# Optimization experiments

Measured on AMD Instinct MI355X. Metric: run time of the kernel, lower is better.

Reference implementation:

```python
import jax, jax.numpy as jnp
import numpy as np

B, T, D = 8, 1024, 512
H = 8
F_OUT = D // H          # 64 per head
ALPHA = 0.2             # LeakyReLU slope in GAT
MASK_RATE = 0.3
GAMMA = 0.0625          # DistanceAdj gamma
BIAS = 0.2              # DistanceAdj bias
LN_EPS = 1e-5
NEG_INF = -9e15
L2_EPS = 1e-12          # F.normalize eps


def setup_inputs() -> dict:
    key = jax.random.key(0)
    ks = jax.random.split(key, 8)
    return {
        "x": jax.random.normal(ks[0], (B, T, D), jnp.float32),
        "W": jax.random.normal(ks[1], (H, D, F_OUT), jnp.float32) * 0.05,
        "a_src": jax.random.normal(ks[2], (H, F_OUT), jnp.float32) * 0.05,
        "a_dst": jax.random.normal(ks[3], (H, F_OUT), jnp.float32) * 0.05,
        "W2": jax.random.normal(ks[4], (D, D), jnp.float32) * 0.02,
        "b2": jnp.zeros((D,), jnp.float32),
        "ln_g": jnp.ones((D,), jnp.float32),
        "ln_b": jnp.zeros((D,), jnp.float32),
    }


def _distance_adj(batch, t):
    # DistanceAdj: Gaussian kernel over temporal index distance, shared across batch
    idx = jnp.arange(t, dtype=jnp.float32)
    d2 = (idx[:, None] - idx[None, :]) ** 2
    adj = jnp.exp(-GAMMA * d2 - BIAS)                      # [T, T]
    return jnp.broadcast_to(adj[None], (batch, t, t))      # [B, T, T]


def reference(x, W, a_src, a_dst, W2, b2, ln_g, ln_b):
    b, t, d = x.shape
    adj = _distance_adj(b, t)

    # top-k magnitude node selection -> row/col union mask (index_fill loop)
    k = int(MASK_RATE * t)
    mags = jnp.linalg.norm(x, axis=2)                      # [B, T]
    _, topk = jax.lax.top_k(mags, k)                       # [B, k]
    sel = jnp.zeros((b, t), bool).at[jnp.arange(b)[:, None], topk].set(True)
    mask = sel[:, :, None] | sel[:, None, :]               # rows OR cols filled
    adj = jnp.where(mask, adj, 0.0)

    # GAT multi-head attention (dense masked form, dropout=0 at eval)
    Wh = jnp.einsum("btd,hdf->bhtf", x, W)                 # [B,H,T,F']
    e_src = jnp.einsum("bhtf,hf->bht", Wh, a_src)
    e_dst = jnp.einsum("bhtf,hf->bht", Wh, a_dst)
    e = jax.nn.leaky_relu(e_src[..., :, None] + e_dst[..., None, :], ALPHA)
    e = jnp.where(adj[:, None] > 0, e, NEG_INF)            # masked logits
    attn = jax.nn.softmax(e, axis=-1)                      # [B,H,T,T]
    hp = jnp.einsum("bhts,bhsf->bhtf", attn, Wh)
    hp = jax.nn.elu(hp)                                    # concat=True -> elu per head
    tmp = hp.transpose(0, 2, 1, 3).reshape(b, t, d)        # concat heads -> [B,T,512]

    # signed-sqrt + F.normalize (default dim=1 -> over T axis)
    tmp = jnp.sqrt(jax.nn.relu(tmp)) - jnp.sqrt(jax.nn.relu(-tmp))
    nrm = jnp.linalg.norm(tmp, axis=1, keepdims=True)      # [B,1,D]
    tmp = tmp / jnp.maximum(nrm, L2_EPS)

    # residual linear + LayerNorm + permute
    y = x + tmp @ W2 + b2
    mu = jnp.mean(y, axis=-1, keepdims=True)
    var = jnp.mean((y - mu) ** 2, axis=-1, keepdims=True)
    y = (y - mu) / jnp.sqrt(var + LN_EPS) * ln_g + ln_b
    return y.transpose(0, 2, 1)                            # [B, D, T]
```

## Files before the change

### kernel.cpp

```cpp
#include <hip/hip_runtime.h>
#include <hip/hip_bf16.h>

typedef unsigned short u16;
typedef short bf16x8 __attribute__((ext_vector_type(8)));
typedef float f32x4 __attribute__((ext_vector_type(4)));
typedef int   i32x4 __attribute__((ext_vector_type(4)));

#define NB 8
#define NT 1024
#define ND 512
#define KSEL 307
#define PSTR 152
#define TSTR 136

__device__ __forceinline__ float bf2f(u16 u){
  union { unsigned int i; float f; } c; c.i = ((unsigned int)u) << 16; return c.f;
}
__device__ __forceinline__ u16 f2bf(float f){
  __hip_bfloat16 h = __float2bfloat16(f);
  u16 u; __builtin_memcpy(&u, &h, 2); return u;
}

__global__ void k_convert_w(const float* __restrict__ W, const float* __restrict__ W2,
                            u16* __restrict__ WcatT, u16* __restrict__ W2T){
  int idx = blockIdx.x * 256 + threadIdx.x;
  if (idx < 262144){
    int c = idx >> 9, d = idx & 511;
    int src = ((c >> 6) << 15) | (d << 6) | (c & 63);
    WcatT[idx] = f2bf(W[src]);
  } else {
    int i = idx - 262144;
    int n = i >> 9, k = i & 511;
    W2T[i] = f2bf(W2[(k << 9) | n]);
  }
}

__global__ void k_select(const float* __restrict__ mags, int* __restrict__ sel){
  __shared__ float sm[NT];
  int b = blockIdx.x;
  int tid = threadIdx.x;
  for (int i = tid; i < NT; i += 256) sm[i] = mags[b * NT + i];
  __syncthreads();
  int tl = tid >> 2, tq = tid & 3;
  int t = blockIdx.y * 64 + tl;
  float m = sm[t];
  int cnt = 0;
  int s0 = tq * 256;
  for (int s = s0; s < s0 + 256; s++){
    float v = sm[s];
    cnt += (v > m) || (v == m && s < t);
  }
  cnt += __shfl_xor(cnt, 1, 64);
  cnt += __shfl_xor(cnt, 2, 64);
  if (tq == 0) sel[b * NT + t] = (cnt < KSEL) ? 1 : 0;
}

__launch_bounds__(256)
__global__ void k_gemm_wh(const float* __restrict__ x, const u16* __restrict__ Bt,
                          const float* __restrict__ a_src, const float* __restrict__ a_dst,
                          u16* __restrict__ WhT, float* __restrict__ es, float* __restrict__ ed,
                          float* __restrict__ mags){
  __shared__ u16 smem[128 * TSTR];
  u16* As = smem;
  u16* Bs = smem + 5120;
  int m0 = blockIdx.x * 128, n0 = blockIdx.y * 128;
  int tid = threadIdx.x;
  int wv = tid >> 6, lane = tid & 63;
  int wr = wv & 1, wc = wv >> 1;
  int quad = lane >> 4, lr = lane & 15;
  f32x4 acc[4][4] = {};
  float sq[2] = {0.f, 0.f};
  for (int kt = 0; kt < 512; kt += 32){
    __syncthreads();
#pragma unroll
    for (int i = 0; i < 2; i++){
      int e = tid * 8 + i * 2048;
      int r = e >> 5, c = e & 31;
      const float* xa = &x[(m0 + r) * 512 + kt + c];
      f32x4 u0 = *(const f32x4*)xa;
      f32x4 u1 = *(const f32x4*)(xa + 4);
      u16 pk[8];
#pragma unroll
      for (int q = 0; q < 4; q++){
        sq[i] += u0[q]*u0[q] + u1[q]*u1[q];
        pk[q] = f2bf(u0[q]); pk[4+q] = f2bf(u1[q]);
      }
      *(bf16x8*)&As[r*40 + c] = *(const bf16x8*)pk;
      *(bf16x8*)&Bs[r*40 + c] = *(const bf16x8*)&Bt[(n0 + r) * 512 + kt + c];
    }
    __syncthreads();
    bf16x8 af[4], bfr[4];
#pragma unroll
    for (int i = 0; i < 4; i++){
      af[i]  = *(const bf16x8*)&As[(wr*64 + i*16 + lr)*40 + quad*8];
      bfr[i] = *(const bf16x8*)&Bs[(wc*64 + i*16 + lr)*40 + quad*8];
    }
#pragma unroll
    for (int mi = 0; mi < 4; mi++)
#pragma unroll
      for (int ni = 0; ni < 4; ni++)
        acc[mi][ni] = __builtin_amdgcn_mfma_f32_16x16x32_bf16(af[mi], bfr[ni], acc[mi][ni], 0, 0, 0);
  }
  if (blockIdx.y == 0){
#pragma unroll
    for (int i = 0; i < 2; i++){
      float s = sq[i];
      s += __shfl_xor(s, 1, 64);
      s += __shfl_xor(s, 2, 64);
      if ((tid & 3) == 0) mags[m0 + i*64 + (tid >> 2)] = sqrtf(s);
    }
  }
  int h = (n0 >> 6) + wc;
  float asv[4], adv[4];
#pragma unroll
  for (int ni = 0; ni < 4; ni++){
    int colg = n0 + wc*64 + ni*16 + lr;
    asv[ni] = a_src[colg & 511];
    adv[ni] = a_dst[colg & 511];
  }
#pragma unroll
  for (int mi = 0; mi < 4; mi++)
#pragma unroll
    for (int r = 0; r < 4; r++){
      float pes = 0.f, ped = 0.f;
#pragma unroll
      for (int ni = 0; ni < 4; ni++){
        pes += acc[mi][ni][r] * asv[ni];
        ped += acc[mi][ni][r] * adv[ni];
      }
#pragma unroll
      for (int mofs = 1; mofs < 16; mofs <<= 1){
        pes += __shfl_xor(pes, mofs, 64);
        ped += __shfl_xor(ped, mofs, 64);
      }
      if (lr == 0){
        int rowg = m0 + wr*64 + mi*16 + quad*4 + r;
        int bb_ = rowg >> 10, tt = rowg & 1023;
        es[(bb_ * 8 + h) * NT + tt] = pes;
        ed[(bb_ * 8 + h) * NT + tt] = ped;
      }
    }
  __syncthreads();
  u16* Tr = smem;
#pragma unroll
  for (int mi = 0; mi < 4; mi++)
#pragma unroll
    for (int ni = 0; ni < 4; ni++){
      int cl = wc*64 + ni*16 + lr;
      int tl = wr*64 + mi*16 + quad*4;
#pragma unroll
      for (int r = 0; r < 4; r++) Tr[cl*TSTR + tl + r] = f2bf(acc[mi][ni][r]);
    }
  __syncthreads();
  int c = tid >> 1, hf = tid & 1;
  int b2_ = m0 >> 10;
  u16* dst = &WhT[(b2_ * 512 + n0 + c) * NT + (m0 & 1023) + hf*64];
  const u16* srcp = &Tr[c*TSTR + hf*64];
#pragma unroll
  for (int k8 = 0; k8 < 8; k8++)
    *(bf16x8*)(dst + k8*8) = *(const bf16x8*)(srcp + k8*8);
}

__launch_bounds__(256)
__global__ void k_attn(const u16* __restrict__ WhT, const float* __restrict__ es,
                       const float* __restrict__ ed, const int* __restrict__ sel,
                       u16* __restrict__ t2b, float* __restrict__ cn){
  __shared__ u16 P[64 * PSTR];
  __shared__ float edw[144];
  __shared__ int   selw[144];
  __shared__ float esw[64];
  __shared__ float swv[64];
  int bh = blockIdx.x;
  int b = bh >> 3;
  int t0 = blockIdx.y * 64;
  int tid = threadIdx.x;
  int wv = tid >> 6, lane = tid & 63;
  int quad = lane >> 4, lr = lane & 15;
  int s_base = t0 - 40;
  for (int i = tid; i < 144; i += 256){
    int s = s_base + i;
    bool ok = (s >= 0 && s < NT);
    edw[i]  = ok ? ed[bh * NT + s] : 0.f;
    selw[i] = ok ? sel[b * NT + s] : 0;
  }
  if (tid < 64) esw[tid] = es[bh * NT + t0 + tid];
  {
    i32x4 z = {};
    for (int i = lane; i < 304; i += 64){
      int r16 = i / 19, c16 = i - r16 * 19;
      *(i32x4*)&P[(16*wv + r16) * PSTR + c16 * 8] = z;
    }
  }
  __syncthreads();
  {
    int tl = 16*wv + (lane >> 2);
    int q = lane & 3;
    float e_t = esw[tl];
    int sel_t = selw[tl + 40];
    float part = 0.f;
    for (int j = q; j <= 80; j += 4){
      int sw = tl + j;
      int s = s_base + sw;
      float w = 0.f;
      if (s >= 0 && s < NT && (sel_t | selw[sw])){
        float v = e_t + edw[sw];
        v = v > 0.f ? v : 0.2f * v;
        v = fminf(v, 60.f);
        w = bf2f(f2bf(__expf(v)));
      }
      part += w;
      if (w != 0.f) P[tl * PSTR + sw] = f2bf(w);
    }
    part += __shfl_xor(part, 1, 64);
    part += __shfl_xor(part, 2, 64);
    if (q == 0) swv[tl] = part;
  }
  f32x4 acc[4] = {};
  const u16* vbase = WhT + (bh * 64) * NT;
#pragma unroll
  for (int ks = 0; ks < 96; ks += 32){
    bf16x8 afr = *(const bf16x8*)&P[(16*wv + lr) * PSTR + 16*wv + ks + quad*8];
    int tb = s_base + 16*wv + ks + quad*8;
    bool ok = (tb >= 0) && (tb < NT);
    bf16x8 zf = {};
#pragma unroll
    for (int jn = 0; jn < 4; jn++){
      bf16x8 bfr = ok ? *(const bf16x8*)&vbase[(16*jn + lr) * NT + tb] : zf;
      acc[jn] = __builtin_amdgcn_mfma_f32_16x16x32_bf16(afr, bfr, acc[jn], 0, 0, 0);
    }
  }
#pragma unroll
  for (int jn = 0; jn < 4; jn++){
    float ssum = 0.f;
#pragma unroll
    for (int r = 0; r < 4; r++){
      int t_loc = 16*wv + quad*4 + r;
      float sw_ = swv[t_loc];
      float hp = acc[jn][r] / (sw_ > 0.f ? sw_ : 1.f);
      hp = hp > 0.f ? hp : (__expf(hp) - 1.f);
      float o = hp >= 0.f ? sqrtf(hp) : -sqrtf(-hp);
      ssum += o * o;
      t2b[(b * NT + t0 + t_loc) * ND + (bh & 7) * 64 + 16*jn + lr] = f2bf(o);
    }
    ssum += __shfl_xor(ssum, 16, 64);
    ssum += __shfl_xor(ssum, 32, 64);
    if (quad == 0) atomicAdd(&cn[b * ND + (bh & 7) * 64 + 16*jn + lr], ssum);
  }
}

__launch_bounds__(256)
__global__ void k_gemm2(const u16* __restrict__ A, const u16* __restrict__ Bt,
                        const float* __restrict__ xres, const float* __restrict__ b2,
                        const float* __restrict__ cn, float* __restrict__ Y,
                        float* __restrict__ rsum, float* __restrict__ rqsum){
  __shared__ u16 As[128 * 40];
  __shared__ u16 Bs[128 * 40];
  __shared__ float scl[512];
  int m0 = blockIdx.x * 128, n0 = blockIdx.y * 128;
  int tid = threadIdx.x;
  int wv = tid >> 6, lane = tid & 63;
  int wr = wv & 1, wc = wv >> 1;
  int quad = lane >> 4, lr = lane & 15;
  int bb0 = (m0 >> 10) << 9;
  for (int i = tid; i < 512; i += 256){
    float nv = sqrtf(cn[bb0 + i]);
    scl[i] = 1.f / fmaxf(nv, 1e-12f);
  }
  f32x4 acc[4][4] = {};
  for (int kt = 0; kt < 512; kt += 32){
    __syncthreads();
#pragma unroll
    for (int i = 0; i < 2; i++){
      int e = tid * 8 + i * 2048;
      int r = e >> 5, c = e & 31;
      bf16x8 raw = *(const bf16x8*)&A[(m0 + r) * 512 + kt + c];
      u16 pk[8];
#pragma unroll
      for (int q = 0; q < 8; q++)
        pk[q] = f2bf(bf2f((u16)raw[q]) * scl[kt + c + q]);
      *(bf16x8*)&As[r*40 + c] = *(const bf16x8*)pk;
      *(bf16x8*)&Bs[r*40 + c] = *(const bf16x8*)&Bt[(n0 + r) * 512 + kt + c];
    }
    __syncthreads();
    bf16x8 af[4], bfr[4];
#pragma unroll
    for (int i = 0; i < 4; i++){
      af[i]  = *(const bf16x8*)&As[(wr*64 + i*16 + lr)*40 + quad*8];
      bfr[i] = *(const bf16x8*)&Bs[(wc*64 + i*16 + lr)*40 + quad*8];
    }
#pragma unroll
    for (int mi = 0; mi < 4; mi++)
#pragma unroll
      for (int ni = 0; ni < 4; ni++)
        acc[mi][ni] = __builtin_amdgcn_mfma_f32_16x16x32_bf16(af[mi], bfr[ni], acc[mi][ni], 0, 0, 0);
  }
  float b2v[4];
#pragma unroll
  for (int ni = 0; ni < 4; ni++) b2v[ni] = b2[n0 + wc*64 + ni*16 + lr];
#pragma unroll
  for (int mi = 0; mi < 4; mi++){
    int rgb = m0 + wr*64 + mi*16 + quad*4;
#pragma unroll
    for (int r = 0; r < 4; r++){
      int row = rgb + r;
      float rs = 0.f, rq = 0.f;
#pragma unroll
      for (int ni = 0; ni < 4; ni++){
        int cg = n0 + wc*64 + ni*16 + lr;
        int idx = row * 512 + cg;
        float yv = acc[mi][ni][r] + xres[idx] + b2v[ni];
        Y[idx] = yv;
        rs += yv; rq += yv * yv;
      }
#pragma unroll
      for (int m2 = 1; m2 < 16; m2 <<= 1){
        rs += __shfl_xor(rs, m2, 64);
        rq += __shfl_xor(rq, m2, 64);
      }
      if (lr == 0){
        atomicAdd(&rsum[row], rs);
        atomicAdd(&rqsum[row], rq);
      }
    }
  }
}

__global__ void k_outln(const float* __restrict__ Y, const float* __restrict__ rsum,
                        const float* __restrict__ rqsum, const float* __restrict__ g,
                        const float* __restrict__ bb, float* __restrict__ out){
  __shared__ float mus[64], rss[64];
  __shared__ float tile[64 * 65];
  int t0 = blockIdx.x * 64, b = blockIdx.y;
  int tid = threadIdx.x;
  if (tid < 64){
    int row = b * NT + t0 + tid;
    float m = rsum[row] * (1.f/512.f);
    float var = rqsum[row] * (1.f/512.f) - m * m;
    mus[tid] = m;
    rss[tid] = 1.f / sqrtf(var + 1e-5f);
  }
  __syncthreads();
  int j = tid & 63, i0 = tid >> 6;
  for (int c0 = 0; c0 < 512; c0 += 64){
#pragma unroll
    for (int k = 0; k < 16; k++){
      int i = i0 + k * 4;
      float v = (Y[(b * NT + t0 + i) * ND + c0 + j] - mus[i]) * rss[i] * g[c0 + j] + bb[c0 + j];
      tile[i * 65 + j] = v;
    }
    __syncthreads();
#pragma unroll
    for (int k = 0; k < 16; k++){
      int jj = i0 + k * 4;
      out[(b * ND + c0 + jj) * NT + t0 + j] = tile[j * 65 + jj];
    }
    __syncthreads();
  }
}

extern "C" void kernel_launch(void* const* d_in, const int* in_sizes, int n_in,
                              void* d_out, int out_size, void* d_ws, size_t ws_size,
                              hipStream_t stream) {
  (void)in_sizes; (void)n_in; (void)out_size; (void)ws_size;
  const float* x     = (const float*)d_in[0];
  const float* W     = (const float*)d_in[1];
  const float* a_src = (const float*)d_in[2];
  const float* a_dst = (const float*)d_in[3];
  const float* W2    = (const float*)d_in[4];
  const float* b2    = (const float*)d_in[5];
  const float* ln_g  = (const float*)d_in[6];
  const float* ln_b  = (const float*)d_in[7];
  char* ws = (char*)d_ws;
  int*   sel   = (int*)  (ws + 256);
  float* mags  = (float*)(ws + 33024);
  u16*   WcatT = (u16*)  (ws + 65792);
  u16*   W2T   = (u16*)  (ws + 590080);
  float* es    = (float*)(ws + 1124608);
  float* ed    = (float*)(ws + 1386752);
  float* cn    = (float*)(ws + 1648896);
  float* rsum  = (float*)(ws + 1665280);
  float* rqsum = (float*)(ws + 1698048);
  u16*   WhT   = (u16*)  (ws + 2097152);
  u16*   t2b   = (u16*)  (ws + 18874368);
  float* Y     = (float*)(ws + 2097152);
  float* out   = (float*)d_out;

  k_convert_w<<<2048, 256, 0, stream>>>(W, W2, WcatT, W2T);
  hipMemsetAsync(cn, 0, 81920, stream);
  k_gemm_wh  <<<dim3(64, 4), 256, 0, stream>>>(x, WcatT, a_src, a_dst, WhT, es, ed, mags);
  k_select   <<<dim3(NB, 16), 256, 0, stream>>>(mags, sel);
  k_attn     <<<dim3(64, 16), 256, 0, stream>>>(WhT, es, ed, sel, t2b, cn);
  k_gemm2    <<<dim3(64, 4), 256, 0, stream>>>(t2b, W2T, x, b2, cn, Y, rsum, rqsum);
  k_outln    <<<dim3(16, NB), 256, 0, stream>>>(Y, rsum, rqsum, ln_g, ln_b, out);
}
```

Measured before the change: 170.0 us.

## Shrink GEMM N-tiles to 64 and split LayerNorm output over channels for more blocks

Both bf16 MFMA GEMMs now use 128x64 tiles with each wave owning 32 rows, which doubles the grid from 256 to 512 blocks and adds a min-3-blocks-per-SM occupancy hint. The Wh GEMM maps one head per block column, so the attention-logit reductions and the transposed write are reorganized. The output LayerNorm transpose kernel is split four ways over channel chunks. The aim is better fill of the 256 CUs on small grids, at the cost of re-reading and re-converting the x/A tiles twice as often in the GEMMs.

```diff
diff --git a/kernel.cpp b/kernel.cpp
--- a/kernel.cpp
+++ b/kernel.cpp
@@ -55,20 +55,20 @@
   if (tq == 0) sel[b * NT + t] = (cnt < KSEL) ? 1 : 0;
 }
 
-__launch_bounds__(256)
+__launch_bounds__(256, 3)
 __global__ void k_gemm_wh(const float* __restrict__ x, const u16* __restrict__ Bt,
                           const float* __restrict__ a_src, const float* __restrict__ a_dst,
                           u16* __restrict__ WhT, float* __restrict__ es, float* __restrict__ ed,
                           float* __restrict__ mags){
-  __shared__ u16 smem[128 * TSTR];
+  __shared__ u16 smem[8704];
   u16* As = smem;
   u16* Bs = smem + 5120;
-  int m0 = blockIdx.x * 128, n0 = blockIdx.y * 128;
+  int m0 = blockIdx.x * 128;
+  int h  = blockIdx.y;
   int tid = threadIdx.x;
   int wv = tid >> 6, lane = tid & 63;
-  int wr = wv & 1, wc = wv >> 1;
   int quad = lane >> 4, lr = lane & 15;
-  f32x4 acc[4][4] = {};
+  f32x4 acc[2][4] = {};
   float sq[2] = {0.f, 0.f};
   for (int kt = 0; kt < 512; kt += 32){
     __syncthreads();
@@ -86,17 +86,20 @@
         pk[q] = f2bf(u0[q]); pk[4+q] = f2bf(u1[q]);
       }
       *(bf16x8*)&As[r*40 + c] = *(const bf16x8*)pk;
-      *(bf16x8*)&Bs[r*40 + c] = *(const bf16x8*)&Bt[(n0 + r) * 512 + kt + c];
-    }
-    __syncthreads();
-    bf16x8 af[4], bfr[4];
-#pragma unroll
-    for (int i = 0; i < 4; i++){
-      af[i]  = *(const bf16x8*)&As[(wr*64 + i*16 + lr)*40 + quad*8];
-      bfr[i] = *(const bf16x8*)&Bs[(wc*64 + i*16 + lr)*40 + quad*8];
-    }
-#pragma unroll
-    for (int mi = 0; mi < 4; mi++)
+    }
+    {
+      int e = tid * 8;
+      int r = e >> 5, c = e & 31;
+      *(bf16x8*)&Bs[r*40 + c] = *(const bf16x8*)&Bt[(h * 64 + r) * 512 + kt + c];
+    }
+    __syncthreads();
+    bf16x8 af[2], bfr[4];
+#pragma unroll
+    for (int i = 0; i < 2; i++) af[i] = *(const bf16x8*)&As[(wv*32 + i*16 + lr)*40 + quad*8];
+#pragma unroll
+    for (int i = 0; i < 4; i++) bfr[i] = *(const bf16x8*)&Bs[(i*16 + lr)*40 + quad*8];
+#pragma unroll
+    for (int mi = 0; mi < 2; mi++)
 #pragma unroll
       for (int ni = 0; ni < 4; ni++)
         acc[mi][ni] = __builtin_amdgcn_mfma_f32_16x16x32_bf16(af[mi], bfr[ni], acc[mi][ni], 0, 0, 0);
@@ -110,16 +113,14 @@
       if ((tid & 3) == 0) mags[m0 + i*64 + (tid >> 2)] = sqrtf(s);
     }
   }
-  int h = (n0 >> 6) + wc;
   float asv[4], adv[4];
 #pragma unroll
   for (int ni = 0; ni < 4; ni++){
-    int colg = n0 + wc*64 + ni*16 + lr;
-    asv[ni] = a_src[colg & 511];
-    adv[ni] = a_dst[colg & 511];
-  }
-#pragma unroll
-  for (int mi = 0; mi < 4; mi++)
+    asv[ni] = a_src[h*64 + ni*16 + lr];
+    adv[ni] = a_dst[h*64 + ni*16 + lr];
+  }
+#pragma unroll
+  for (int mi = 0; mi < 2; mi++)
 #pragma unroll
     for (int r = 0; r < 4; r++){
       float pes = 0.f, ped = 0.f;
@@ -134,7 +135,7 @@
         ped += __shfl_xor(ped, mofs, 64);
       }
       if (lr == 0){
-        int rowg = m0 + wr*64 + mi*16 + quad*4 + r;
+        int rowg = m0 + wv*32 + mi*16 + quad*4 + r;
         int bb_ = rowg >> 10, tt = rowg & 1023;
         es[(bb_ * 8 + h) * NT + tt] = pes;
         ed[(bb_ * 8 + h) * NT + tt] = ped;
@@ -143,21 +144,21 @@
   __syncthreads();
   u16* Tr = smem;
 #pragma unroll
-  for (int mi = 0; mi < 4; mi++)
+  for (int mi = 0; mi < 2; mi++)
 #pragma unroll
     for (int ni = 0; ni < 4; ni++){
-      int cl = wc*64 + ni*16 + lr;
-      int tl = wr*64 + mi*16 + quad*4;
-#pragma unroll
-      for (int r = 0; r < 4; r++) Tr[cl*TSTR + tl + r] = f2bf(acc[mi][ni][r]);
-    }
-  __syncthreads();
-  int c = tid >> 1, hf = tid & 1;
-  int b2_ = m0 >> 10;
-  u16* dst = &WhT[(b2_ * 512 + n0 + c) * NT + (m0 & 1023) + hf*64];
-  const u16* srcp = &Tr[c*TSTR + hf*64];
-#pragma unroll
-  for (int k8 = 0; k8 < 8; k8++)
+      int fl = ni*16 + lr;
+      int tl = wv*32 + mi*16 + quad*4;
+#pragma unroll
+      for (int r = 0; r < 4; r++) Tr[fl*TSTR + tl + r] = f2bf(acc[mi][ni][r]);
+    }
+  __syncthreads();
+  int f = tid >> 2, seg = tid & 3;
+  int b_ = m0 >> 10;
+  u16* dst = &WhT[(b_ * 512 + h * 64 + f) * NT + (m0 & 1023) + seg*32];
+  const u16* srcp = &Tr[f*TSTR + seg*32];
+#pragma unroll
+  for (int k8 = 0; k8 < 4; k8++)
     *(bf16x8*)(dst + k8*8) = *(const bf16x8*)(srcp + k8*8);
 }
 
@@ -248,25 +249,24 @@
   }
 }
 
-__launch_bounds__(256)
+__launch_bounds__(256, 3)
 __global__ void k_gemm2(const u16* __restrict__ A, const u16* __restrict__ Bt,
                         const float* __restrict__ xres, const float* __restrict__ b2,
                         const float* __restrict__ cn, float* __restrict__ Y,
                         float* __restrict__ rsum, float* __restrict__ rqsum){
   __shared__ u16 As[128 * 40];
-  __shared__ u16 Bs[128 * 40];
+  __shared__ u16 Bs[64 * 40];
   __shared__ float scl[512];
-  int m0 = blockIdx.x * 128, n0 = blockIdx.y * 128;
+  int m0 = blockIdx.x * 128, n0 = blockIdx.y * 64;
   int tid = threadIdx.x;
   int wv = tid >> 6, lane = tid & 63;
-  int wr = wv & 1, wc = wv >> 1;
   int quad = lane >> 4, lr = lane & 15;
   int bb0 = (m0 >> 10) << 9;
   for (int i = tid; i < 512; i += 256){
     float nv = sqrtf(cn[bb0 + i]);
     scl[i] = 1.f / fmaxf(nv, 1e-12f);
   }
-  f32x4 acc[4][4] = {};
+  f32x4 acc[2][4] = {};
   for (int kt = 0; kt < 512; kt += 32){
     __syncthreads();
 #pragma unroll
@@ -279,34 +279,37 @@
       for (int q = 0; q < 8; q++)
         pk[q] = f2bf(bf2f((u16)raw[q]) * scl[kt + c + q]);
       *(bf16x8*)&As[r*40 + c] = *(const bf16x8*)pk;
+    }
+    {
+      int e = tid * 8;
+      int r = e >> 5, c = e & 31;
       *(bf16x8*)&Bs[r*40 + c] = *(const bf16x8*)&Bt[(n0 + r) * 512 + kt + c];
     }
     __syncthreads();
-    bf16x8 af[4], bfr[4];
-#pragma unroll
-    for (int i = 0; i < 4; i++){
-      af[i]  = *(const bf16x8*)&As[(wr*64 + i*16 + lr)*40 + quad*8];
-      bfr[i] = *(const bf16x8*)&Bs[(wc*64 + i*16 + lr)*40 + quad*8];
-    }
-#pragma unroll
-    for (int mi = 0; mi < 4; mi++)
+    bf16x8 af[2], bfr[4];
+#pragma unroll
+    for (int i = 0; i < 2; i++) af[i] = *(const bf16x8*)&As[(wv*32 + i*16 + lr)*40 + quad*8];
+#pragma unroll
+    for (int i = 0; i < 4; i++) bfr[i] = *(const bf16x8*)&Bs[(i*16 + lr)*40 + quad*8];
+#pragma unroll
+    for (int mi = 0; mi < 2; mi++)
 #pragma unroll
       for (int ni = 0; ni < 4; ni++)
         acc[mi][ni] = __builtin_amdgcn_mfma_f32_16x16x32_bf16(af[mi], bfr[ni], acc[mi][ni], 0, 0, 0);
   }
   float b2v[4];
 #pragma unroll
-  for (int ni = 0; ni < 4; ni++) b2v[ni] = b2[n0 + wc*64 + ni*16 + lr];
-#pragma unroll
-  for (int mi = 0; mi < 4; mi++){
-    int rgb = m0 + wr*64 + mi*16 + quad*4;
+  for (int ni = 0; ni < 4; ni++) b2v[ni] = b2[n0 + ni*16 + lr];
+#pragma unroll
+  for (int mi = 0; mi < 2; mi++){
+    int rgb = m0 + wv*32 + mi*16 + quad*4;
 #pragma unroll
     for (int r = 0; r < 4; r++){
       int row = rgb + r;
       float rs = 0.f, rq = 0.f;
 #pragma unroll
       for (int ni = 0; ni < 4; ni++){
-        int cg = n0 + wc*64 + ni*16 + lr;
+        int cg = n0 + ni*16 + lr;
         int idx = row * 512 + cg;
         float yv = acc[mi][ni][r] + xres[idx] + b2v[ni];
         Y[idx] = yv;
@@ -331,6 +334,7 @@
   __shared__ float mus[64], rss[64];
   __shared__ float tile[64 * 65];
   int t0 = blockIdx.x * 64, b = blockIdx.y;
+  int cbase = blockIdx.z * 128;
   int tid = threadIdx.x;
   if (tid < 64){
     int row = b * NT + t0 + tid;
@@ -341,7 +345,7 @@
   }
   __syncthreads();
   int j = tid & 63, i0 = tid >> 6;
-  for (int c0 = 0; c0 < 512; c0 += 64){
+  for (int c0 = cbase; c0 < cbase + 128; c0 += 64){
 #pragma unroll
     for (int k = 0; k < 16; k++){
       int i = i0 + k * 4;
@@ -387,9 +391,9 @@
 
   k_convert_w<<<2048, 256, 0, stream>>>(W, W2, WcatT, W2T);
   hipMemsetAsync(cn, 0, 81920, stream);
-  k_gemm_wh  <<<dim3(64, 4), 256, 0, stream>>>(x, WcatT, a_src, a_dst, WhT, es, ed, mags);
+  k_gemm_wh  <<<dim3(64, 8), 256, 0, stream>>>(x, WcatT, a_src, a_dst, WhT, es, ed, mags);
   k_select   <<<dim3(NB, 16), 256, 0, stream>>>(mags, sel);
   k_attn     <<<dim3(64, 16), 256, 0, stream>>>(WhT, es, ed, sel, t2b, cn);
-  k_gemm2    <<<dim3(64, 4), 256, 0, stream>>>(t2b, W2T, x, b2, cn, Y, rsum, rqsum);
-  k_outln    <<<dim3(16, NB), 256, 0, stream>>>(Y, rsum, rqsum, ln_g, ln_b, out);
-}
+  k_gemm2    <<<dim3(64, 8), 256, 0, stream>>>(t2b, W2T, x, b2, cn, Y, rsum, rqsum);
+  k_outln    <<<dim3(16, NB, 4), 256, 0, stream>>>(Y, rsum, rqsum, ln_g, ln_b, out);
+}
```

Result: faster. 161.1 us (median of 2 runs) (-5.2%).
